# Kernel optimization log

Measured on AMD Instinct MI355X. Metric: run time of the kernel, lower is better.

## Reference

```python
import jax, jax.numpy as jnp
import numpy as np
import math

SEQ_LEN = 2048
D_MODEL = 1024
N_HEAD = 16
BATCH = 4


def setup_inputs() -> dict:
    key = jax.random.key(0)
    ks = jax.random.split(key, 12)
    D, T = D_MODEL, SEQ_LEN
    lin_bound = 1.0 / math.sqrt(D)  # torch nn.Linear default init
    xav_bound = math.sqrt(6.0 / (T + T))  # xavier_uniform for wbias
    u = lambda k, shape, b: jax.random.uniform(k, shape, jnp.float32, -b, b)
    return {
        "x": jax.random.normal(ks[0], (BATCH, T, D), jnp.float32),
        "dummy": 0,
        "Wq": u(ks[1], (D, D), lin_bound), "bq": u(ks[2], (D,), lin_bound),
        "Wk": u(ks[3], (D, D), lin_bound), "bk": u(ks[4], (D,), lin_bound),
        "Wv": u(ks[5], (D, D), lin_bound), "bv": u(ks[6], (D,), lin_bound),
        "Wo": u(ks[7], (D, D), lin_bound), "bo": u(ks[8], (D,), lin_bound),
        "wbias": u(ks[9], (T, T), xav_bound),
    }


def reference(x, dummy, Wq, bq, Wk, bk, Wv, bv, Wo, bo, wbias):
    B, T, D = x.shape
    H = N_HEAD
    dh = D // H

    def proj(W, b):
        # nn.Linear: x @ W.T + b, then view(B,T,H,dh) -> (B,H,T,dh)
        y = jnp.einsum('btd,ed->bte', x, W) + b
        return y.reshape(B, T, H, dh).transpose(0, 2, 1, 3)

    Q = proj(Wq, bq)
    K = proj(Wk, bk)
    V = proj(Wv, bv)

    ew = jnp.exp(wbias[:T, :T])          # [T,T] (unstabilized, as in torch src)
    eK = jnp.exp(K)                      # [B,H,T,dh]
    numer = jnp.einsum('ts,bhsd->bhtd', ew, eK * V)
    denom = jnp.einsum('ts,bhsd->bhtd', ew, eK)
    out = jax.nn.sigmoid(Q) * (numer / denom)   # [B,H,T,dh]
    out = out.transpose(0, 2, 1, 3).reshape(B, T, D)
    return jnp.einsum('btd,ed->bte', out, Wo) + bo
```

## Files before the change

kernel.cpp:

```cpp
#include <hip/hip_runtime.h>
#include <stdint.h>

typedef unsigned short u16;
typedef __attribute__((ext_vector_type(8))) short short8;
typedef __attribute__((ext_vector_type(4))) float f32x4;

#define SEQ 2048
#define DM 1024
#define NB 4
#define ROWS (NB*SEQ)

__device__ __forceinline__ u16 f2bf(float f) {
  union { float f; uint32_t u; } x; x.f = f;
  uint32_t u = x.u;
  uint32_t r = u + 0x7FFFu + ((u >> 16) & 1u);
  return (u16)(r >> 16);
}
__device__ __forceinline__ float bf2f(u16 h) {
  union { uint32_t u; float f; } x; x.u = ((uint32_t)h) << 16;
  return x.f;
}

__device__ __forceinline__ void g2l16(void* lds, const void* g) {
  __builtin_amdgcn_global_load_lds(
      (const __attribute__((address_space(1))) void*)g,
      (__attribute__((address_space(3))) void*)lds, 16, 0, 0);
}

template<int MODE>
__global__ void k_cvt(const float* __restrict__ in, u16* __restrict__ out, int n4) {
  int i = blockIdx.x * 256 + threadIdx.x;
  if (i >= n4) return;
  float4 v = reinterpret_cast<const float4*>(in)[i];
  if (MODE == 1) { v.x = __expf(v.x); v.y = __expf(v.y); v.z = __expf(v.z); v.w = __expf(v.w); }
  ushort4 o;
  o.x = f2bf(v.x); o.y = f2bf(v.y); o.z = f2bf(v.z); o.w = f2bf(v.w);
  reinterpret_cast<ushort4*>(out)[i] = o;
}

#define STAGE(t_, bf_) do { \
  _Pragma("unroll") for (int c = 0; c < 4; ++c) { \
    int idx = c * 512 + tid; \
    int r = idx >> 3; \
    int ce = ((idx & 7) ^ (r & 7)) * 8; \
    g2l16(&lds[(bf_)*BUFE + idx*8], Ag + (long)r*KD + (t_)*64 + ce); \
  } \
  _Pragma("unroll") for (int c = 0; c < BN/64; ++c) { \
    int idx = c * 512 + tid; \
    int r = idx >> 3; \
    int ce = ((idx & 7) ^ (r & 7)) * 8; \
    g2l16(&lds[(bf_)*BUFE + 16384 + idx*8], Bg + (long)r*KD + (t_)*64 + ce); \
  } } while (0)

#define LDA8(mh_) do { \
  _Pragma("unroll") for (int i = 0; i < FM/2; ++i) \
  _Pragma("unroll") for (int k = 0; k < 2; ++k) \
    a[i][k] = *(const short8*)&lds[ab + ((mh_)*(RW/2) + i*16 + lr)*64 + 8*(((k<<2)|kg) ^ (lr&7))]; \
  } while (0)

#define LDB8(nh_) do { \
  _Pragma("unroll") for (int j = 0; j < 2; ++j) \
  _Pragma("unroll") for (int k = 0; k < 2; ++k) \
    bn[nh_][j][k] = *(const short8*)&lds[bb + (((nh_)*2+j)*16 + lr)*64 + 8*(((k<<2)|kg) ^ (lr&7))]; \
  } while (0)

#define MM8(mh_, nh_) do { \
  asm volatile("s_waitcnt lgkmcnt(0)" ::: "memory"); \
  __builtin_amdgcn_sched_barrier(0); \
  __builtin_amdgcn_s_setprio(1); \
  _Pragma("unroll") for (int i = 0; i < FM/2; ++i) \
  _Pragma("unroll") for (int j = 0; j < 2; ++j) \
  _Pragma("unroll") for (int k = 0; k < 2; ++k) \
    acc[(mh_)*(FM/2)+i][(nh_)*2+j] = __builtin_amdgcn_mfma_f32_16x16x32_bf16( \
        a[i][k], bn[nh_][j][k], acc[(mh_)*(FM/2)+i][(nh_)*2+j], 0, 0, 0); \
  __builtin_amdgcn_s_setprio(0); \
  } while (0)

template<int KD, int WM, int MODE>
__global__ __launch_bounds__(512)
void k_big(const u16* __restrict__ A, const u16* __restrict__ B,
           void* __restrict__ Cv,
           const float* __restrict__ b0, const float* __restrict__ b1,
           const float* __restrict__ b2, long sB, long sC)
{
  constexpr int WN = 8 / WM;
  constexpr int BN = WN * 64;
  constexpr int RW = 256 / WM;
  constexpr int FM = RW / 16;
  constexpr int NT = KD / 64;
  constexpr int BUFE = (256 + BN) * 64;
  __shared__ u16 lds[2 * BUFE];
  const int tid = threadIdx.x;
  const int l  = tid & 63, wid = tid >> 6;
  const int wm = wid / WN, wn = wid % WN;
  const int lr = l & 15,  kg = l >> 4;
  const int brow = blockIdx.y * 256;
  const int bcol = blockIdx.x * BN;
  const u16* Ag = A + (long)brow * KD;
  const u16* Bg = B + (long)blockIdx.z * sB + (long)bcol * KD;

  f32x4 acc[FM][4];
#pragma unroll
  for (int m = 0; m < FM; ++m)
#pragma unroll
    for (int n = 0; n < 4; ++n) acc[m][n] = (f32x4){0.f, 0.f, 0.f, 0.f};

  short8 a[FM/2][2], bn[2][2][2];

  STAGE(0, 0);
  STAGE(1, 1);

  for (int t = 0; t < NT; ++t) {
    const int bf = t & 1;
    if (t == NT - 1)              asm volatile("s_waitcnt vmcnt(0)" ::: "memory");
    else if constexpr (BN == 256) asm volatile("s_waitcnt vmcnt(8)" ::: "memory");
    else                          asm volatile("s_waitcnt vmcnt(6)" ::: "memory");
    __builtin_amdgcn_s_barrier();
    __builtin_amdgcn_sched_barrier(0);
    const int ab = bf*BUFE + wm*RW*64;
    const int bb = bf*BUFE + 16384 + wn*64*64;
    LDA8(0); LDB8(0); MM8(0, 0);
    LDB8(1);          MM8(0, 1);
    LDA8(1);          MM8(1, 1);
                      MM8(1, 0);
    __builtin_amdgcn_sched_barrier(0);
    __builtin_amdgcn_s_barrier();
    __builtin_amdgcn_sched_barrier(0);
    if (t + 2 < NT) STAGE(t + 2, bf);
  }

#pragma unroll
  for (int m = 0; m < FM; ++m)
#pragma unroll
    for (int n = 0; n < 4; ++n)
#pragma unroll
      for (int r = 0; r < 4; ++r) {
        int row = brow + wm*RW + m*16 + kg*4 + r;
        int col = bcol + wn*64 + n*16 + lr;
        float v = acc[m][n][r];
        if (MODE == 0) {
          ((float*)Cv)[(long)blockIdx.z * sC + (long)row * 2048 + col] = v;
        } else if (MODE == 1) {
          int seg = col >> 10, colr = col & 1023;
          const float* bp = (seg == 0) ? b0 : (seg == 1) ? b1 : b2;
          v += bp[colr];
          if (seg == 0) v = 1.f / (1.f + __expf(-v));
          ((u16*)Cv)[(long)seg * 8388608 + (long)row * 1024 + colr] = f2bf(v);
        } else {
          ((float*)Cv)[(long)row * 1024 + col] = v + b0[col];
        }
      }
}

__global__ void k_trans(const u16* __restrict__ Kb, const u16* __restrict__ Vb,
                        u16* __restrict__ Z) {
  __shared__ u16 lk[64][65];
  __shared__ u16 lv[64][65];
  int s0 = blockIdx.x * 64, e0 = blockIdx.y * 64, b = blockIdx.z;
  int tx = threadIdx.x & 63, ty = threadIdx.x >> 6;
  const long baseIn = (long)b * SEQ * DM;
  for (int j = ty; j < 64; j += 4) {
    lk[j][tx] = Kb[baseIn + (long)(s0 + j) * DM + e0 + tx];
    lv[j][tx] = Vb[baseIn + (long)(s0 + j) * DM + e0 + tx];
  }
  __syncthreads();
  const long ob = (long)b * 2 * DM * SEQ;
  for (int j = ty; j < 64; j += 4) {
    int e = e0 + j;
    float kf = bf2f(lk[tx][j]);
    float vf = bf2f(lv[tx][j]);
    float ek = __expf(kf);
    Z[ob + (long)e * SEQ + s0 + tx]        = f2bf(ek * vf);
    Z[ob + (long)(DM + e) * SEQ + s0 + tx] = f2bf(ek);
  }
}

__global__ void k_combine(const u16* __restrict__ Qs, const float* __restrict__ R,
                          u16* __restrict__ out1) {
  long i4 = (long)blockIdx.x * 256 + threadIdx.x;
  if (i4 >= (long)ROWS * DM / 4) return;
  long i = i4 * 4;
  int e = (int)(i & (DM - 1));
  long row = i >> 10;
  float4 nu = *(const float4*)&R[row * (2 * DM) + e];
  float4 de = *(const float4*)&R[row * (2 * DM) + DM + e];
  ushort4 q = *(const ushort4*)&Qs[i];
  ushort4 o;
  o.x = f2bf(bf2f(q.x) * nu.x / de.x);
  o.y = f2bf(bf2f(q.y) * nu.y / de.y);
  o.z = f2bf(bf2f(q.z) * nu.z / de.z);
  o.w = f2bf(bf2f(q.w) * nu.w / de.w);
  *(ushort4*)&out1[i] = o;
}

extern "C" void kernel_launch(void* const* d_in, const int* in_sizes, int n_in,
                              void* d_out, int out_size, void* d_ws, size_t ws_size,
                              hipStream_t stream)
{
  const float* x     = (const float*)d_in[0];
  const float* Wq    = (const float*)d_in[2];
  const float* bq    = (const float*)d_in[3];
  const float* Wk    = (const float*)d_in[4];
  const float* bk    = (const float*)d_in[5];
  const float* Wv    = (const float*)d_in[6];
  const float* bv    = (const float*)d_in[7];
  const float* Wo    = (const float*)d_in[8];
  const float* bo    = (const float*)d_in[9];
  const float* wbias = (const float*)d_in[10];

  char* ws = (char*)d_ws;
  u16*  xb  = (u16*)(ws);
  u16*  Wqb = (u16*)(ws + 16777216);
  u16*  Wkb = Wqb + 1024 * 1024;
  u16*  Wvb = Wkb + 1024 * 1024;
  u16*  Wob = Wvb + 1024 * 1024;
  u16*  EW  = (u16*)(ws + 25165824);
  u16*  Qs  = (u16*)(ws + 33554432);
  u16*  Kb  = (u16*)(ws + 50331648);
  u16*  Vb  = (u16*)(ws + 67108864);
  u16*  Z   = (u16*)(ws + 83886080);
  float* R  = (float*)(ws + 117440512);
  u16*  out1 = xb;

  k_cvt<0><<<ROWS * DM / 4 / 256, 256, 0, stream>>>(x, xb, ROWS * DM / 4);
  k_cvt<0><<<DM * DM / 4 / 256, 256, 0, stream>>>(Wq, Wqb, DM * DM / 4);
  k_cvt<0><<<DM * DM / 4 / 256, 256, 0, stream>>>(Wk, Wkb, DM * DM / 4);
  k_cvt<0><<<DM * DM / 4 / 256, 256, 0, stream>>>(Wv, Wvb, DM * DM / 4);
  k_cvt<0><<<DM * DM / 4 / 256, 256, 0, stream>>>(Wo, Wob, DM * DM / 4);
  k_cvt<1><<<SEQ * SEQ / 4 / 256, 256, 0, stream>>>(wbias, EW, SEQ * SEQ / 4);

  dim3 gqkv(3072 / 128, ROWS / 256, 1);
  k_big<1024, 4, 1><<<gqkv, 512, 0, stream>>>(xb, Wqb, Qs, bq, bk, bv, 0, 0);

  dim3 gt(SEQ / 64, DM / 64, NB);
  k_trans<<<gt, 256, 0, stream>>>(Kb, Vb, Z);

  dim3 g8(8, 8, NB);
  k_big<2048, 2, 0><<<g8, 512, 0, stream>>>(EW, Z, R, nullptr, nullptr, nullptr,
                                            (long)2 * DM * SEQ, (long)SEQ * 2 * DM);

  k_combine<<<ROWS * DM / 4 / 256, 256, 0, stream>>>(Qs, R, out1);

  dim3 gop(DM / 128, ROWS / 256, 1);
  k_big<1024, 4, 2><<<gop, 512, 0, stream>>>(out1, Wob, (float*)d_out, bo, nullptr,
                                             nullptr, 0, 0);
}
```

Baseline: 321.9 us.

## Fuse numer/denom combine into EW GEMM epilogue and merge conversion kernels

```diff
diff --git a/kernel.cpp b/kernel.cpp
--- a/kernel.cpp
+++ b/kernel.cpp
@@ -27,15 +27,22 @@
       (__attribute__((address_space(3))) void*)lds, 16, 0, 0);
 }
 
-template<int MODE>
-__global__ void k_cvt(const float* __restrict__ in, u16* __restrict__ out, int n4) {
+__global__ void k_cvt_all(const float* __restrict__ x,
+                          const float* __restrict__ Wq, const float* __restrict__ Wk,
+                          const float* __restrict__ Wv, const float* __restrict__ Wo,
+                          const float* __restrict__ wb, u16* __restrict__ dws) {
   int i = blockIdx.x * 256 + threadIdx.x;
-  if (i >= n4) return;
-  float4 v = reinterpret_cast<const float4*>(in)[i];
-  if (MODE == 1) { v.x = __expf(v.x); v.y = __expf(v.y); v.z = __expf(v.z); v.w = __expf(v.w); }
-  ushort4 o;
-  o.x = f2bf(v.x); o.y = f2bf(v.y); o.z = f2bf(v.z); o.w = f2bf(v.w);
-  reinterpret_cast<ushort4*>(out)[i] = o;
+  const float* src; long dst; bool ex = false;
+  if (i < 2097152) { src = x + (long)i * 4; dst = (long)i * 4; }
+  else if (i < 3145728) {
+    int j = i - 2097152, which = j >> 18, o = j & 262143;
+    const float* Wp = (which == 0) ? Wq : (which == 1) ? Wk : (which == 2) ? Wv : Wo;
+    src = Wp + (long)o * 4; dst = 8388608 + (long)(j) * 4;
+  } else { int j = i - 3145728; src = wb + (long)j * 4; dst = 12582912 + (long)j * 4; ex = true; }
+  float4 v = *(const float4*)src;
+  if (ex) { v.x = __expf(v.x); v.y = __expf(v.y); v.z = __expf(v.z); v.w = __expf(v.w); }
+  ushort4 o4; o4.x = f2bf(v.x); o4.y = f2bf(v.y); o4.z = f2bf(v.z); o4.w = f2bf(v.w);
+  *(ushort4*)(dws + dst) = o4;
 }
 
 #define STAGE(t_, bf_) do { \
@@ -49,7 +56,8 @@
     int idx = c * 512 + tid; \
     int r = idx >> 3; \
     int ce = ((idx & 7) ^ (r & 7)) * 8; \
-    g2l16(&lds[(bf_)*BUFE + 16384 + idx*8], Bg + (long)r*KD + (t_)*64 + ce); \
+    const u16* bp_ = (MODE == 3 && c >= 2) ? (Bg + 896L*KD) : Bg; \
+    g2l16(&lds[(bf_)*BUFE + 16384 + idx*8], bp_ + (long)r*KD + (t_)*64 + ce); \
   } } while (0)
 
 #define LDA8(mh_) do { \
@@ -60,9 +68,11 @@
 
 #define LDB8(nh_) do { \
   _Pragma("unroll") for (int j = 0; j < 2; ++j) \
-  _Pragma("unroll") for (int k = 0; k < 2; ++k) \
-    bn[nh_][j][k] = *(const short8*)&lds[bb + (((nh_)*2+j)*16 + lr)*64 + 8*(((k<<2)|kg) ^ (lr&7))]; \
-  } while (0)
+  _Pragma("unroll") for (int k = 0; k < 2; ++k) { \
+    int rowB_ = (MODE == 3) ? ((nh_)*128 + wn*32 + j*16 + lr) \
+                            : (wn*64 + ((nh_)*2+j)*16 + lr); \
+    bn[nh_][j][k] = *(const short8*)&lds[bb + rowB_*64 + 8*(((k<<2)|kg) ^ (lr&7))]; \
+  } } while (0)
 
 #define MM8(mh_, nh_) do { \
   asm volatile("s_waitcnt lgkmcnt(0)" ::: "memory"); \
@@ -95,7 +105,7 @@
   const int wm = wid / WN, wn = wid % WN;
   const int lr = l & 15,  kg = l >> 4;
   const int brow = blockIdx.y * 256;
-  const int bcol = blockIdx.x * BN;
+  const int bcol = blockIdx.x * ((MODE == 3) ? 128 : BN);
   const u16* Ag = A + (long)brow * KD;
   const u16* Bg = B + (long)blockIdx.z * sB + (long)bcol * KD;
 
@@ -118,7 +128,7 @@
     __builtin_amdgcn_s_barrier();
     __builtin_amdgcn_sched_barrier(0);
     const int ab = bf*BUFE + wm*RW*64;
-    const int bb = bf*BUFE + 16384 + wn*64*64;
+    const int bb = bf*BUFE + 16384;
     LDA8(0); LDB8(0); MM8(0, 0);
     LDB8(1);          MM8(0, 1);
     LDA8(1);          MM8(1, 1);
@@ -129,27 +139,44 @@
     if (t + 2 < NT) STAGE(t + 2, bf);
   }
 
-#pragma unroll
-  for (int m = 0; m < FM; ++m)
-#pragma unroll
-    for (int n = 0; n < 4; ++n)
-#pragma unroll
-      for (int r = 0; r < 4; ++r) {
-        int row = brow + wm*RW + m*16 + kg*4 + r;
-        int col = bcol + wn*64 + n*16 + lr;
-        float v = acc[m][n][r];
-        if (MODE == 0) {
-          ((float*)Cv)[(long)blockIdx.z * sC + (long)row * 2048 + col] = v;
-        } else if (MODE == 1) {
-          int seg = col >> 10, colr = col & 1023;
-          const float* bp = (seg == 0) ? b0 : (seg == 1) ? b1 : b2;
-          v += bp[colr];
-          if (seg == 0) v = 1.f / (1.f + __expf(-v));
-          ((u16*)Cv)[(long)seg * 8388608 + (long)row * 1024 + colr] = f2bf(v);
-        } else {
-          ((float*)Cv)[(long)row * 1024 + col] = v + b0[col];
+  if constexpr (MODE == 3) {
+    const u16* QsP = (const u16*)b0;
+    u16* O = (u16*)Cv;
+    const long rb = (long)blockIdx.z * 2048;
+#pragma unroll
+    for (int m = 0; m < FM; ++m)
+#pragma unroll
+      for (int j = 0; j < 2; ++j)
+#pragma unroll
+        for (int r = 0; r < 4; ++r) {
+          int row = brow + wm*RW + m*16 + kg*4 + r;
+          int e = bcol + wn*32 + j*16 + lr;
+          float nu = acc[m][j][r];
+          float de = acc[m][2+j][r];
+          float q = bf2f(QsP[(rb + row) * 1024 + e]);
+          O[(rb + row) * 1024 + e] = f2bf(q * nu * __builtin_amdgcn_rcpf(de));
         }
-      }
+  } else {
+#pragma unroll
+    for (int m = 0; m < FM; ++m)
+#pragma unroll
+      for (int n = 0; n < 4; ++n)
+#pragma unroll
+        for (int r = 0; r < 4; ++r) {
+          int row = brow + wm*RW + m*16 + kg*4 + r;
+          int col = bcol + wn*64 + n*16 + lr;
+          float v = acc[m][n][r];
+          if (MODE == 1) {
+            int seg = col >> 10, colr = col & 1023;
+            const float* bp = (seg == 0) ? b0 : (seg == 1) ? b1 : b2;
+            v += bp[colr];
+            if (seg == 0) v = 1.f / (1.f + __expf(-v));
+            ((u16*)Cv)[(long)seg * 8388608 + (long)row * 1024 + colr] = f2bf(v);
+          } else {
+            ((float*)Cv)[(long)row * 1024 + col] = v + b0[col];
+          }
+        }
+  }
 }
 
 __global__ void k_trans(const u16* __restrict__ Kb, const u16* __restrict__ Vb,
@@ -173,24 +200,6 @@
     Z[ob + (long)e * SEQ + s0 + tx]        = f2bf(ek * vf);
     Z[ob + (long)(DM + e) * SEQ + s0 + tx] = f2bf(ek);
   }
-}
-
-__global__ void k_combine(const u16* __restrict__ Qs, const float* __restrict__ R,
-                          u16* __restrict__ out1) {
-  long i4 = (long)blockIdx.x * 256 + threadIdx.x;
-  if (i4 >= (long)ROWS * DM / 4) return;
-  long i = i4 * 4;
-  int e = (int)(i & (DM - 1));
-  long row = i >> 10;
-  float4 nu = *(const float4*)&R[row * (2 * DM) + e];
-  float4 de = *(const float4*)&R[row * (2 * DM) + DM + e];
-  ushort4 q = *(const ushort4*)&Qs[i];
-  ushort4 o;
-  o.x = f2bf(bf2f(q.x) * nu.x / de.x);
-  o.y = f2bf(bf2f(q.y) * nu.y / de.y);
-  o.z = f2bf(bf2f(q.z) * nu.z / de.z);
-  o.w = f2bf(bf2f(q.w) * nu.w / de.w);
-  *(ushort4*)&out1[i] = o;
 }
 
 extern "C" void kernel_launch(void* const* d_in, const int* in_sizes, int n_in,
@@ -211,23 +220,15 @@
   char* ws = (char*)d_ws;
   u16*  xb  = (u16*)(ws);
   u16*  Wqb = (u16*)(ws + 16777216);
-  u16*  Wkb = Wqb + 1024 * 1024;
-  u16*  Wvb = Wkb + 1024 * 1024;
-  u16*  Wob = Wvb + 1024 * 1024;
+  u16*  Wob = (u16*)(ws + 16777216 + 3 * 2097152);
   u16*  EW  = (u16*)(ws + 25165824);
   u16*  Qs  = (u16*)(ws + 33554432);
   u16*  Kb  = (u16*)(ws + 50331648);
   u16*  Vb  = (u16*)(ws + 67108864);
   u16*  Z   = (u16*)(ws + 83886080);
-  float* R  = (float*)(ws + 117440512);
   u16*  out1 = xb;
 
-  k_cvt<0><<<ROWS * DM / 4 / 256, 256, 0, stream>>>(x, xb, ROWS * DM / 4);
-  k_cvt<0><<<DM * DM / 4 / 256, 256, 0, stream>>>(Wq, Wqb, DM * DM / 4);
-  k_cvt<0><<<DM * DM / 4 / 256, 256, 0, stream>>>(Wk, Wkb, DM * DM / 4);
-  k_cvt<0><<<DM * DM / 4 / 256, 256, 0, stream>>>(Wv, Wvb, DM * DM / 4);
-  k_cvt<0><<<DM * DM / 4 / 256, 256, 0, stream>>>(Wo, Wob, DM * DM / 4);
-  k_cvt<1><<<SEQ * SEQ / 4 / 256, 256, 0, stream>>>(wbias, EW, SEQ * SEQ / 4);
+  k_cvt_all<<<16384, 256, 0, stream>>>(x, Wq, Wk, Wv, Wo, wbias, (u16*)ws);
 
   dim3 gqkv(3072 / 128, ROWS / 256, 1);
   k_big<1024, 4, 1><<<gqkv, 512, 0, stream>>>(xb, Wqb, Qs, bq, bk, bv, 0, 0);
@@ -236,10 +237,9 @@
   k_trans<<<gt, 256, 0, stream>>>(Kb, Vb, Z);
 
   dim3 g8(8, 8, NB);
-  k_big<2048, 2, 0><<<g8, 512, 0, stream>>>(EW, Z, R, nullptr, nullptr, nullptr,
-                                            (long)2 * DM * SEQ, (long)SEQ * 2 * DM);
-
-  k_combine<<<ROWS * DM / 4 / 256, 256, 0, stream>>>(Qs, R, out1);
+  k_big<2048, 2, 3><<<g8, 512, 0, stream>>>(EW, Z, out1, (const float*)Qs,
+                                            nullptr, nullptr,
+                                            (long)2 * DM * SEQ, 0);
 
   dim3 gop(DM / 128, ROWS / 256, 1);
   k_big<1024, 4, 2><<<gop, 512, 0, stream>>>(out1, Wob, (float*)d_out, bo, nullptr,
```

Measured after the change: 288.3 us. 1.12x faster.
